# Kernel tuning notes

Measured on AMD Instinct MI355X. Metric: run time of the kernel, lower is better.

The kernel has to match this reference:

```python
import jax, jax.numpy as jnp
import numpy as np

IN_SHAPE = 640
LEVELS = [3, 4, 5]          # pyramid_levels [3,5] expanded
REG_LEN = 64
NUM_CLASSES = 80
MAX_OUT = 100
SCORE_TH = 0.3
IOU_TH = 0.5
NEG_INF = -1e30


def _make_anchors():
    """Anchor-free anchors: one box per grid cell, grid_zero_start=True,
    anchor_scale=1, aspect_ratio=1 -> half-size = stride/2. Normalized by input size."""
    all_a = []
    for lvl in LEVELS:
        stride = 2 ** lvl
        fs = IN_SHAPE // stride
        hh = np.arange(fs, dtype='float32') * stride
        ww = np.arange(fs, dtype='float32') * stride
        wg, hg = np.meshgrid(ww, hh)
        centers = np.stack([hg, wg], -1).reshape(-1, 2)  # [fs*fs, 2] (h, w)
        half = stride * 0.5
        all_a.append(np.concatenate([centers - half, centers + half], -1))
    return np.concatenate(all_a, 0) / IN_SHAPE  # [8400, 4]


def setup_inputs() -> dict:
    key = jax.random.key(0)
    preds = jax.random.normal(key, (64, 8400, REG_LEN + NUM_CLASSES), dtype=jnp.float32)
    anchors = jnp.asarray(_make_anchors(), dtype=jnp.float32)
    return {"preds": preds, "anchors": anchors}


def _decode_yolov8(preds, anchors):
    bbox_logits, cls_logits = preds[..., :REG_LEN], preds[..., REG_LEN:]
    B, N = bbox_logits.shape[:2]
    bins = REG_LEN // 4  # 16
    d = bbox_logits.reshape(B, N, 4, bins)
    # softmax-weighted DFL expectation over bins
    d = jnp.sum(jax.nn.softmax(d, axis=-1) * jnp.arange(bins, dtype=d.dtype), axis=-1)  # [B,N,4]
    tl, br = d[..., :2], d[..., 2:]
    anchors_hw = anchors[:, 2:] - anchors[:, :2]          # [N,2]
    anchors_ctr = (anchors[:, :2] + anchors[:, 2:]) * 0.5  # [N,2]
    bc = (br - tl) * 0.5 * anchors_hw + anchors_ctr        # center
    bhw = (br + tl) * anchors_hw                           # height/width
    boxes = jnp.concatenate([bc - bhw * 0.5, bc + bhw * 0.5], -1)  # [B,N,4] corners
    return boxes, cls_logits


def _iou_one_vs_all(box, boxes):
    tl = jnp.maximum(box[:2], boxes[:, :2])
    br = jnp.minimum(box[2:], boxes[:, 2:])
    inter = jnp.prod(jnp.clip(br - tl, 0.0, None), -1)
    a1 = jnp.prod(box[2:] - box[:2])
    a2 = jnp.prod(boxes[:, 2:] - boxes[:, :2], -1)
    return inter / (a1 + a2 - inter + 1e-9)


def _nms_single(boxes, scores):
    """Greedy hard NMS for one image. boxes [N,4], scores [N] -> idxs [MAX_OUT] (-1 = invalid)."""
    n = scores.shape[0]
    sc0 = jnp.where(scores > SCORE_TH, scores, NEG_INF)

    def step(sc, _):
        j = jnp.argmax(sc)
        valid = sc[j] > NEG_INF * 0.5
        idx = jnp.where(valid, j, -1).astype(jnp.int32)
        iou = _iou_one_vs_all(boxes[j], boxes)
        sc = jnp.where((iou > IOU_TH) | (jnp.arange(n) == j), NEG_INF, sc)
        return sc, idx

    _, idxs = jax.lax.scan(step, sc0, None, length=MAX_OUT)
    return idxs


def reference(preds, anchors):
    boxes, cls = _decode_yolov8(preds, anchors)       # [B,N,4], [B,N,C]
    scores = jnp.max(cls, -1)                          # [B,N]
    labels = jnp.argmax(cls, -1).astype(jnp.int32)     # [B,N]
    idxs = jax.vmap(_nms_single)(boxes, scores)        # [B,MAX_OUT]
    valid = idxs >= 0
    safe = jnp.maximum(idxs, 0)
    out_boxes = jnp.take_along_axis(boxes, safe[:, :, None], axis=1) * valid[..., None]
    out_scores = jnp.take_along_axis(scores, safe, axis=1) * valid
    out_labels = jnp.where(valid, jnp.take_along_axis(labels, safe, axis=1), -1)
    return out_boxes, out_labels, out_scores
```

## Files before the change

kernel.cpp:

```cpp
#include <hip/hip_runtime.h>

namespace {
constexpr int kB = 64;
constexpr int kN = 8400;
constexpr int kMain = 8192;
constexpr int kTail = kN - kMain;
constexpr int kReg = 64;
constexpr int kCls = 80;
constexpr int kStride = kReg + kCls;
constexpr int kMaxOut = 100;
constexpr float kScoreTh = 0.3f;
constexpr float kIouTh = 0.5f;
}

__global__ __launch_bounds__(256) void decode2_k(
    const float* __restrict__ preds,
    const float* __restrict__ anchors,
    float4* __restrict__ boxes,
    float* __restrict__ scores,
    int* __restrict__ labels,
    unsigned long long* __restrict__ keys)
{
    __shared__ float lds[64 * 148];
    const int tid = threadIdx.x;
    const size_t gbase = (size_t)blockIdx.x * 64;

    const float4* src = (const float4*)(preds + gbase * kStride);
    float4* l4 = (float4*)lds;
#pragma unroll
    for (int k = 0; k < 9; ++k) {
        int i = tid + k * 256;
        int row = i / 36, col = i - row * 36;
        l4[row * 37 + col] = src[i];
    }
    __syncthreads();

    const int a = tid >> 2, s = tid & 3;
    const float* rowp = lds + a * 148;

    float x[16];
    const float4* q = (const float4*)(rowp + s * 16);
#pragma unroll
    for (int j = 0; j < 4; ++j) ((float4*)x)[j] = q[j];
    float m = x[0];
#pragma unroll
    for (int j = 1; j < 16; ++j) m = fmaxf(m, x[j]);
    float se = 0.f, we = 0.f;
#pragma unroll
    for (int j = 0; j < 16; ++j) {
        float t = expf(x[j] - m);
        se += t;
        we += t * (float)j;
    }
    float d = we / se;

    const float4* cl = (const float4*)(rowp + kReg + s * 20);
    float bv = -3e38f; int bi = 0;
#pragma unroll
    for (int c = 0; c < 5; ++c) {
        float4 v = cl[c];
        int cb = s * 20 + 4 * c;
        if (v.x > bv) { bv = v.x; bi = cb; }
        if (v.y > bv) { bv = v.y; bi = cb + 1; }
        if (v.z > bv) { bv = v.z; bi = cb + 2; }
        if (v.w > bv) { bv = v.w; bi = cb + 3; }
    }

    const int lane = tid & 63;
    const int base = lane & ~3;
    float d0 = __shfl(d, base + 0, 64);
    float d1 = __shfl(d, base + 1, 64);
    float d2 = __shfl(d, base + 2, 64);
    float d3 = __shfl(d, base + 3, 64);
    float v1 = __shfl(bv, base + 1, 64); int i1 = __shfl(bi, base + 1, 64);
    float v2 = __shfl(bv, base + 2, 64); int i2 = __shfl(bi, base + 2, 64);
    float v3 = __shfl(bv, base + 3, 64); int i3 = __shfl(bi, base + 3, 64);

    if (s == 0) {
        float best = bv; int bl = bi;
        if (v1 > best) { best = v1; bl = i1; }
        if (v2 > best) { best = v2; bl = i2; }
        if (v3 > best) { best = v3; bl = i3; }

        size_t gi = gbase + a;
        int bimg = (int)(gi / kN);
        int n = (int)(gi - (size_t)bimg * kN);
        float4 av = ((const float4*)anchors)[n];
        float ah0 = av.z - av.x, ah1 = av.w - av.y;
        float c0 = (av.x + av.z) * 0.5f, c1 = (av.y + av.w) * 0.5f;
        float bc0 = (d2 - d0) * 0.5f * ah0 + c0;
        float bc1 = (d3 - d1) * 0.5f * ah1 + c1;
        float bh0 = (d2 + d0) * ah0;
        float bh1 = (d3 + d1) * ah1;
        boxes[gi] = make_float4(bc0 - bh0 * 0.5f, bc1 - bh1 * 0.5f,
                                bc0 + bh0 * 0.5f, bc1 + bh1 * 0.5f);
        scores[gi] = best;
        labels[gi] = bl;

        unsigned long long kkey = ~0ULL;
        if (best > kScoreTh) {
            unsigned u = __float_as_uint(best);
            unsigned o = u ^ ((u & 0x80000000u) ? 0xFFFFFFFFu : 0x80000000u);
            kkey = ((unsigned long long)(~o) << 32) | (unsigned)n;
        }
        keys[((size_t)bimg << 14) + n] = kkey;
    }
}

__global__ __launch_bounds__(512) void sortL_k(unsigned long long* __restrict__ keys)
{
    __shared__ unsigned long long lk[2048];
    const int img = blockIdx.x >> 2, seg = blockIdx.x & 3;
    const int gofs = seg << 11;
    unsigned long long* base = keys + ((size_t)img << 14) + gofs;

    for (int t = threadIdx.x; t < 2048; t += 512) lk[t] = base[t];
    __syncthreads();
    for (int size = 2; size <= 2048; size <<= 1) {
        for (int stride = size >> 1; stride > 0; stride >>= 1) {
#pragma unroll
            for (int p = 0; p < 2; ++p) {
                int n = threadIdx.x + (p << 9);
                int i = ((n & ~(stride - 1)) << 1) | (n & (stride - 1));
                int j = i + stride;
                bool desc = ((gofs + i) & size) != 0;
                unsigned long long a = lk[i], c = lk[j];
                bool sw = desc ? (c > a) : (a > c);
                if (sw) { lk[i] = c; lk[j] = a; }
            }
            __syncthreads();
        }
    }
    for (int t = threadIdx.x; t < 2048; t += 512) base[t] = lk[t];
}

__global__ __launch_bounds__(256) void gce_k(unsigned long long* __restrict__ keys)
{
    int tg = blockIdx.x * 256 + threadIdx.x;
    int img = tg >> 12;
    int n = tg & 4095;
    unsigned long long* base = keys + ((size_t)img << 14);
    unsigned long long a = base[n], c = base[n + 4096];
    if (a > c) { base[n] = c; base[n + 4096] = a; }
}

template <int SIZE>
__global__ __launch_bounds__(512) void lm2_k(unsigned long long* __restrict__ keys)
{
    __shared__ unsigned long long lk[4096];
    const int img = blockIdx.x >> 1, half = blockIdx.x & 1;
    const int gofs = half << 12;
    unsigned long long* base = keys + ((size_t)img << 14) + gofs;

    for (int t = threadIdx.x; t < 4096; t += 512) lk[t] = base[t];
    __syncthreads();
    const bool desc = (gofs & SIZE) != 0;
    for (int stride = 2048; stride > 0; stride >>= 1) {
#pragma unroll
        for (int p = 0; p < 4; ++p) {
            int n = threadIdx.x + (p << 9);
            int i = ((n & ~(stride - 1)) << 1) | (n & (stride - 1));
            int j = i + stride;
            unsigned long long a = lk[i], c = lk[j];
            bool sw = desc ? (c > a) : (a > c);
            if (sw) { lk[i] = c; lk[j] = a; }
        }
        __syncthreads();
    }
    for (int t = threadIdx.x; t < 4096; t += 512) base[t] = lk[t];
}

__device__ __forceinline__ unsigned long long getB_(
    const unsigned long long* tailL, int p1, int x)
{
    int t = p1 + x;
    return (t < 256) ? tailL[t] : ~0ULL;
}

__global__ __launch_bounds__(256) void nms_k(
    const float4* __restrict__ boxes,
    const float* __restrict__ scores,
    const int* __restrict__ labels,
    const unsigned long long* __restrict__ keys,
    float* __restrict__ out)
{
    __shared__ unsigned long long tailL[256];
    __shared__ unsigned long long aw[512];
    __shared__ float4 sbox[256];
    __shared__ float  sar[256];
    __shared__ int    sidx[256];
    __shared__ float4 kboxL[kMaxOut];
    __shared__ float  kareaL[kMaxOut];
    __shared__ int    kidxL[kMaxOut];
    __shared__ unsigned long long ballS[4];
    __shared__ int p0S, p1S, kcS, doneS, stopS;

    const int b = blockIdx.x, tid = threadIdx.x;
    const unsigned long long* mainA = keys + ((size_t)b << 14);
    const float4* bx = boxes + (size_t)b * kN;

    if (tid == 0) { p0S = 0; p1S = 0; kcS = 0; doneS = 0; }

    tailL[tid] = (tid < kTail) ? mainA[kMain + tid] : ~0ULL;
    __syncthreads();
    for (int size = 2; size <= 256; size <<= 1) {
        for (int stride = size >> 1; stride > 0; stride >>= 1) {
            if (tid < 128) {
                int i = ((tid & ~(stride - 1)) << 1) | (tid & (stride - 1));
                int j = i + stride;
                bool desc = (i & size) != 0;
                unsigned long long a = tailL[i], c = tailL[j];
                bool sw = desc ? (c > a) : (a > c);
                if (sw) { tailL[i] = c; tailL[j] = a; }
            }
            __syncthreads();
        }
    }

    int kc = 0;
    for (int c = 0; c < 33; ++c) {
        int p0 = p0S, p1 = p1S;
        aw[tid]       = (p0 + tid       < kMain) ? mainA[p0 + tid]       : ~0ULL;
        aw[tid + 256] = (p0 + tid + 256 < kMain) ? mainA[p0 + tid + 256] : ~0ULL;
        __syncthreads();

        int d = tid;
        int lo = 0, hi = d;
        while (lo < hi) {
            int mid = (lo + hi) >> 1;
            bool c2 = getB_(tailL, p1, d - mid - 1) < aw[mid];
            if (c2) hi = mid; else lo = mid + 1;
        }
        unsigned long long av = aw[lo];
        unsigned long long bv = getB_(tailL, p1, d - lo);
        unsigned long long key = (av <= bv) ? av : bv;

        bool alive = (key != ~0ULL);
        int idx = alive ? (int)(key & 0xFFFFFFFFULL) : 0;
        float4 cb = bx[idx];
        float ac = (cb.z - cb.x) * (cb.w - cb.y);

        if (alive) {
            for (int k = 0; k < kc; ++k) {
                float4 kb = kboxL[k];
                float t0 = fmaxf(kb.x, cb.x), t1 = fmaxf(kb.y, cb.y);
                float b0 = fminf(kb.z, cb.z), b1 = fminf(kb.w, cb.w);
                float inter = fmaxf(b0 - t0, 0.f) * fmaxf(b1 - t1, 0.f);
                float iou = inter / (kareaL[k] + ac - inter + 1e-9f);
                if (iou > kIouTh) { alive = false; break; }
            }
        }
        sbox[tid] = cb; sar[tid] = ac; sidx[tid] = idx;
        unsigned long long mm = __ballot((int)alive);
        if ((tid & 63) == 0) ballS[tid >> 6] = mm;
        if (tid == 0) {
            stopS = (key == ~0ULL);
            int lo2 = 0, hi2 = 256;
            while (lo2 < hi2) {
                int mid = (lo2 + hi2) >> 1;
                bool c2 = getB_(tailL, p1, 255 - mid) < aw[mid];
                if (c2) hi2 = mid; else lo2 = mid + 1;
            }
            p0S = p0 + lo2; p1S = p1 + (256 - lo2);
        }
        __syncthreads();
        if (stopS) break;

        if (tid < 64) {
            const int lane = tid;
            unsigned a4 = 0;
#pragma unroll
            for (int j = 0; j < 4; ++j)
                a4 |= (unsigned)((ballS[j] >> lane) & 1ULL) << j;
            int kcl = kc;
            while (true) {
                int jF = -1, lF = 0;
#pragma unroll
                for (int j = 0; j < 4; ++j) {
                    if (jF < 0) {
                        unsigned long long m2 = __ballot((int)((a4 >> j) & 1u));
                        if (m2) { jF = j; lF = __ffsll((unsigned long long)m2) - 1; }
                    }
                }
                if (jF < 0) break;
                int cs = (jF << 6) + lF;
                float4 kb = sbox[cs];
                float kar = sar[cs];
                if (lane == 0) {
                    kboxL[kcl] = kb; kareaL[kcl] = kar; kidxL[kcl] = sidx[cs];
                }
                if (lane == lF) a4 &= ~(1u << jF);
                ++kcl;
                if (kcl == kMaxOut) break;
#pragma unroll
                for (int j = 0; j < 4; ++j) {
                    if ((a4 >> j) & 1u) {
                        float4 cb2 = sbox[lane + (j << 6)];
                        float ac2 = sar[lane + (j << 6)];
                        float t0 = fmaxf(kb.x, cb2.x), t1 = fmaxf(kb.y, cb2.y);
                        float b0 = fminf(kb.z, cb2.z), b1 = fminf(kb.w, cb2.w);
                        float inter = fmaxf(b0 - t0, 0.f) * fmaxf(b1 - t1, 0.f);
                        float iou = inter / (kar + ac2 - inter + 1e-9f);
                        if (iou > kIouTh) a4 &= ~(1u << j);
                    }
                }
            }
            if (lane == 0) { kcS = kcl; if (kcl == kMaxOut) doneS = 1; }
        }
        __syncthreads();
        kc = kcS;
        if (doneS) break;
    }

    int kcf = kcS;
    if (tid < kMaxOut) {
        if (tid < kcf) {
            int idx = kidxL[tid];
            ((float4*)out)[b * kMaxOut + tid] = kboxL[tid];
            out[kB * kMaxOut * 4 + b * kMaxOut + tid] =
                (float)labels[(size_t)b * kN + idx];
            out[kB * kMaxOut * 5 + b * kMaxOut + tid] =
                scores[(size_t)b * kN + idx];
        } else {
            ((float4*)out)[b * kMaxOut + tid] = make_float4(0.f, 0.f, 0.f, 0.f);
            out[kB * kMaxOut * 4 + b * kMaxOut + tid] = -1.0f;
            out[kB * kMaxOut * 5 + b * kMaxOut + tid] = 0.0f;
        }
    }
}

extern "C" void kernel_launch(void* const* d_in, const int* in_sizes, int n_in,
                              void* d_out, int out_size, void* d_ws, size_t ws_size,
                              hipStream_t stream)
{
    const float* preds = (const float*)d_in[0];
    const float* anchors = (const float*)d_in[1];
    float* out = (float*)d_out;

    char* ws = (char*)d_ws;
    float4* boxes = (float4*)ws;
    float* scores = (float*)(ws + (size_t)kB * kN * 16);
    int* labels = (int*)(ws + (size_t)kB * kN * 20);
    unsigned long long* keys =
        (unsigned long long*)(ws + (size_t)kB * kN * 24);

    decode2_k<<<(kB * kN) / 64, 256, 0, stream>>>(preds, anchors, boxes, scores, labels, keys);
    sortL_k<<<kB * 4, 512, 0, stream>>>(keys);
    lm2_k<4096><<<kB * 2, 512, 0, stream>>>(keys);
    gce_k<<<(kB * 4096) / 256, 256, 0, stream>>>(keys);
    lm2_k<8192><<<kB * 2, 512, 0, stream>>>(keys);
    nms_k<<<kB, 256, 0, stream>>>(boxes, scores, labels, keys, out);
}
```

Measured before the change: 512.8 us.

## Precompute merged sorted keys and widen NMS to 512-candidate chunks

The final global compare-exchange step is folded into the last bitonic merge kernel, so one launch is removed. The tail merge with the 208 leftover keys moves out of the NMS loop into a separate merge-path kernel that writes a fully sorted key array. NMS then reads 512 candidates per chunk with 512 threads and no per-chunk binary search. The wave-level suppression uses an 8-bit mask per lane with padded shared-memory layout and a shuffle to find the next keeper. This costs an extra workspace buffer and an extra global pass over the keys.

```diff
diff --git a/kernel.cpp b/kernel.cpp
--- a/kernel.cpp
+++ b/kernel.cpp
@@ -9,6 +9,7 @@
 constexpr int kCls = 80;
 constexpr int kStride = kReg + kCls;
 constexpr int kMaxOut = 100;
+constexpr int kM2 = 8704;
 constexpr float kScoreTh = 0.3f;
 constexpr float kIouTh = 0.5f;
 }
@@ -134,18 +135,7 @@
     for (int t = threadIdx.x; t < 2048; t += 512) base[t] = lk[t];
 }
 
-__global__ __launch_bounds__(256) void gce_k(unsigned long long* __restrict__ keys)
-{
-    int tg = blockIdx.x * 256 + threadIdx.x;
-    int img = tg >> 12;
-    int n = tg & 4095;
-    unsigned long long* base = keys + ((size_t)img << 14);
-    unsigned long long a = base[n], c = base[n + 4096];
-    if (a > c) { base[n] = c; base[n + 4096] = a; }
-}
-
-template <int SIZE>
-__global__ __launch_bounds__(512) void lm2_k(unsigned long long* __restrict__ keys)
+__global__ __launch_bounds__(512) void lm4_k(unsigned long long* __restrict__ keys)
 {
     __shared__ unsigned long long lk[4096];
     const int img = blockIdx.x >> 1, half = blockIdx.x & 1;
@@ -154,7 +144,7 @@
 
     for (int t = threadIdx.x; t < 4096; t += 512) lk[t] = base[t];
     __syncthreads();
-    const bool desc = (gofs & SIZE) != 0;
+    const bool desc = (gofs & 4096) != 0;
     for (int stride = 2048; stride > 0; stride >>= 1) {
 #pragma unroll
         for (int p = 0; p < 4; ++p) {
@@ -170,38 +160,46 @@
     for (int t = threadIdx.x; t < 4096; t += 512) base[t] = lk[t];
 }
 
-__device__ __forceinline__ unsigned long long getB_(
-    const unsigned long long* tailL, int p1, int x)
-{
-    int t = p1 + x;
-    return (t < 256) ? tailL[t] : ~0ULL;
-}
-
-__global__ __launch_bounds__(256) void nms_k(
-    const float4* __restrict__ boxes,
-    const float* __restrict__ scores,
-    const int* __restrict__ labels,
+__global__ __launch_bounds__(512) void lm8f_k(
     const unsigned long long* __restrict__ keys,
-    float* __restrict__ out)
+    unsigned long long* __restrict__ keysM)
+{
+    __shared__ unsigned long long lk[4096];
+    const int img = blockIdx.x >> 1, half = blockIdx.x & 1;
+    const unsigned long long* base = keys + ((size_t)img << 14);
+
+    for (int t = threadIdx.x; t < 4096; t += 512) {
+        unsigned long long a = base[t], c = base[t + 4096];
+        lk[t] = half ? (a > c ? a : c) : (a > c ? c : a);
+    }
+    __syncthreads();
+    for (int stride = 2048; stride > 0; stride >>= 1) {
+#pragma unroll
+        for (int p = 0; p < 4; ++p) {
+            int n = threadIdx.x + (p << 9);
+            int i = ((n & ~(stride - 1)) << 1) | (n & (stride - 1));
+            int j = i + stride;
+            unsigned long long a = lk[i], c = lk[j];
+            if (a > c) { lk[i] = c; lk[j] = a; }
+        }
+        __syncthreads();
+    }
+    unsigned long long* dst = keysM + ((size_t)img << 13) + ((size_t)half << 12);
+    for (int t = threadIdx.x; t < 4096; t += 512) dst[t] = lk[t];
+}
+
+__global__ __launch_bounds__(512) void mergeT_k(
+    const unsigned long long* __restrict__ keysM,
+    const unsigned long long* __restrict__ keys,
+    unsigned long long* __restrict__ keys2)
 {
     __shared__ unsigned long long tailL[256];
-    __shared__ unsigned long long aw[512];
-    __shared__ float4 sbox[256];
-    __shared__ float  sar[256];
-    __shared__ int    sidx[256];
-    __shared__ float4 kboxL[kMaxOut];
-    __shared__ float  kareaL[kMaxOut];
-    __shared__ int    kidxL[kMaxOut];
-    __shared__ unsigned long long ballS[4];
-    __shared__ int p0S, p1S, kcS, doneS, stopS;
-
     const int b = blockIdx.x, tid = threadIdx.x;
-    const unsigned long long* mainA = keys + ((size_t)b << 14);
-    const float4* bx = boxes + (size_t)b * kN;
-
-    if (tid == 0) { p0S = 0; p1S = 0; kcS = 0; doneS = 0; }
-
-    tailL[tid] = (tid < kTail) ? mainA[kMain + tid] : ~0ULL;
+    const unsigned long long* A = keysM + ((size_t)b << 13);
+    unsigned long long* dst = keys2 + (size_t)b * kM2;
+
+    if (tid < 256)
+        tailL[tid] = (tid < kTail) ? keys[((size_t)b << 14) + kMain + tid] : ~0ULL;
     __syncthreads();
     for (int size = 2; size <= 256; size <<= 1) {
         for (int stride = size >> 1; stride > 0; stride >>= 1) {
@@ -217,24 +215,49 @@
         }
     }
 
+    const int d0 = tid * 17;
+    int lo = d0 - 256; lo = lo < 0 ? 0 : (lo > kMain ? kMain : lo);
+    int hi = d0 > kMain ? kMain : d0;
+    while (lo < hi) {
+        int mid = (lo + hi) >> 1;
+        if (tailL[d0 - mid - 1] < A[mid]) hi = mid; else lo = mid + 1;
+    }
+    int ai = lo, bi = d0 - lo;
+#pragma unroll
+    for (int k = 0; k < 17; ++k) {
+        unsigned long long av = (ai < kMain) ? A[ai] : ~0ULL;
+        unsigned long long bv = (bi < 256) ? tailL[bi] : ~0ULL;
+        unsigned long long v;
+        if (av <= bv) { v = av; ++ai; } else { v = bv; ++bi; }
+        dst[d0 + k] = v;
+    }
+}
+
+__global__ __launch_bounds__(512) void nms_k(
+    const float4* __restrict__ boxes,
+    const float* __restrict__ scores,
+    const int* __restrict__ labels,
+    const unsigned long long* __restrict__ keys2,
+    float* __restrict__ out)
+{
+    __shared__ float4 sboxT[576];
+    __shared__ float  sarT[576];
+    __shared__ int    sidxT[576];
+    __shared__ float4 kboxL[kMaxOut];
+    __shared__ float  kareaL[kMaxOut];
+    __shared__ int    kidxL[kMaxOut];
+    __shared__ unsigned long long ballS[8];
+    __shared__ int kcS, doneS, stopS;
+
+    const int b = blockIdx.x, tid = threadIdx.x;
+    const unsigned long long* src = keys2 + (size_t)b * kM2;
+    const float4* bx = boxes + (size_t)b * kN;
+
+    if (tid == 0) { kcS = 0; doneS = 0; }
+
     int kc = 0;
-    for (int c = 0; c < 33; ++c) {
-        int p0 = p0S, p1 = p1S;
-        aw[tid]       = (p0 + tid       < kMain) ? mainA[p0 + tid]       : ~0ULL;
-        aw[tid + 256] = (p0 + tid + 256 < kMain) ? mainA[p0 + tid + 256] : ~0ULL;
-        __syncthreads();
-
-        int d = tid;
-        int lo = 0, hi = d;
-        while (lo < hi) {
-            int mid = (lo + hi) >> 1;
-            bool c2 = getB_(tailL, p1, d - mid - 1) < aw[mid];
-            if (c2) hi = mid; else lo = mid + 1;
-        }
-        unsigned long long av = aw[lo];
-        unsigned long long bv = getB_(tailL, p1, d - lo);
-        unsigned long long key = (av <= bv) ? av : bv;
-
+    for (int c = 0; c < 17; ++c) {
+        unsigned long long key = src[(c << 9) + tid];
         bool alive = (key != ~0ULL);
         int idx = alive ? (int)(key & 0xFFFFFFFFULL) : 0;
         float4 cb = bx[idx];
@@ -250,62 +273,46 @@
                 if (iou > kIouTh) { alive = false; break; }
             }
         }
-        sbox[tid] = cb; sar[tid] = ac; sidx[tid] = idx;
+        const int sl = ((tid >> 3) * 9) + (tid & 7);
+        sboxT[sl] = cb; sarT[sl] = ac; sidxT[sl] = idx;
         unsigned long long mm = __ballot((int)alive);
         if ((tid & 63) == 0) ballS[tid >> 6] = mm;
-        if (tid == 0) {
-            stopS = (key == ~0ULL);
-            int lo2 = 0, hi2 = 256;
-            while (lo2 < hi2) {
-                int mid = (lo2 + hi2) >> 1;
-                bool c2 = getB_(tailL, p1, 255 - mid) < aw[mid];
-                if (c2) hi2 = mid; else lo2 = mid + 1;
-            }
-            p0S = p0 + lo2; p1S = p1 + (256 - lo2);
-        }
+        if (tid == 0) stopS = (key == ~0ULL);
         __syncthreads();
         if (stopS) break;
 
         if (tid < 64) {
-            const int lane = tid;
-            unsigned a4 = 0;
-#pragma unroll
-            for (int j = 0; j < 4; ++j)
-                a4 |= (unsigned)((ballS[j] >> lane) & 1ULL) << j;
+            const int l = tid;
+            unsigned a8 = (unsigned)((ballS[l >> 3] >> ((l & 7) << 3)) & 0xFFULL);
             int kcl = kc;
             while (true) {
-                int jF = -1, lF = 0;
-#pragma unroll
-                for (int j = 0; j < 4; ++j) {
-                    if (jF < 0) {
-                        unsigned long long m2 = __ballot((int)((a4 >> j) & 1u));
-                        if (m2) { jF = j; lF = __ffsll((unsigned long long)m2) - 1; }
-                    }
-                }
-                if (jF < 0) break;
-                int cs = (jF << 6) + lF;
-                float4 kb = sbox[cs];
-                float kar = sar[cs];
-                if (lane == 0) {
-                    kboxL[kcl] = kb; kareaL[kcl] = kar; kidxL[kcl] = sidx[cs];
-                }
-                if (lane == lF) a4 &= ~(1u << jF);
+                unsigned long long m = __ballot(a8 != 0);
+                if (!m) break;
+                int lf = __ffsll(m) - 1;
+                unsigned af = (unsigned)__shfl((int)a8, lf, 64);
+                int jf = __ffs((int)af) - 1;
+                int ks = lf * 9 + jf;
+                float4 kb = sboxT[ks];
+                float kar = sarT[ks];
+                if (l == 0) { kboxL[kcl] = kb; kareaL[kcl] = kar; kidxL[kcl] = sidxT[ks]; }
+                if (l == lf) a8 &= ~(1u << jf);
                 ++kcl;
                 if (kcl == kMaxOut) break;
 #pragma unroll
-                for (int j = 0; j < 4; ++j) {
-                    if ((a4 >> j) & 1u) {
-                        float4 cb2 = sbox[lane + (j << 6)];
-                        float ac2 = sar[lane + (j << 6)];
+                for (int j = 0; j < 8; ++j) {
+                    if ((a8 >> j) & 1u) {
+                        int sj = l * 9 + j;
+                        float4 cb2 = sboxT[sj];
+                        float ac2 = sarT[sj];
                         float t0 = fmaxf(kb.x, cb2.x), t1 = fmaxf(kb.y, cb2.y);
                         float b0 = fminf(kb.z, cb2.z), b1 = fminf(kb.w, cb2.w);
                         float inter = fmaxf(b0 - t0, 0.f) * fmaxf(b1 - t1, 0.f);
                         float iou = inter / (kar + ac2 - inter + 1e-9f);
-                        if (iou > kIouTh) a4 &= ~(1u << j);
+                        if (iou > kIouTh) a8 &= ~(1u << j);
                     }
                 }
             }
-            if (lane == 0) { kcS = kcl; if (kcl == kMaxOut) doneS = 1; }
+            if (l == 0) { kcS = kcl; if (kcl == kMaxOut) doneS = 1; }
         }
         __syncthreads();
         kc = kcS;
@@ -343,11 +350,14 @@
     int* labels = (int*)(ws + (size_t)kB * kN * 20);
     unsigned long long* keys =
         (unsigned long long*)(ws + (size_t)kB * kN * 24);
+    unsigned long long* keysM =
+        (unsigned long long*)(ws + (size_t)kB * kN * 24 + (size_t)kB * 16384 * 8);
+    unsigned long long* keys2 = keysM + (size_t)kB * kMain;
 
     decode2_k<<<(kB * kN) / 64, 256, 0, stream>>>(preds, anchors, boxes, scores, labels, keys);
     sortL_k<<<kB * 4, 512, 0, stream>>>(keys);
-    lm2_k<4096><<<kB * 2, 512, 0, stream>>>(keys);
-    gce_k<<<(kB * 4096) / 256, 256, 0, stream>>>(keys);
-    lm2_k<8192><<<kB * 2, 512, 0, stream>>>(keys);
-    nms_k<<<kB, 256, 0, stream>>>(boxes, scores, labels, keys, out);
-}
+    lm4_k<<<kB * 2, 512, 0, stream>>>(keys);
+    lm8f_k<<<kB * 2, 512, 0, stream>>>(keys, keysM);
+    mergeT_k<<<kB, 512, 0, stream>>>(keysM, keys, keys2);
+    nms_k<<<kB, 512, 0, stream>>>(boxes, scores, labels, keys2, out);
+}
```

Measured after the change: 565.1 us. +10.2%, slower.

## Keep bitonic sort keys in registers with wave shuffles and LDS exchange

Applied to the files above, without the earlier changes.

The bitonic sort and merge kernels now keep 4 or 8 keys per thread in registers. Strides within a thread are handled in registers, strides within a wavefront use __shfl_xor, and only large strides exchange through LDS, each with a pair of barriers. This removes most LDS traffic and the barrier after every stride. The cost is higher register pressure and more complex index logic that has to match the original sort direction exactly.

```diff
diff --git a/kernel.cpp b/kernel.cpp
--- a/kernel.cpp
+++ b/kernel.cpp
@@ -110,28 +110,71 @@
 __global__ __launch_bounds__(512) void sortL_k(unsigned long long* __restrict__ keys)
 {
     __shared__ unsigned long long lk[2048];
+    const int tid = threadIdx.x;
     const int img = blockIdx.x >> 2, seg = blockIdx.x & 3;
     const int gofs = seg << 11;
     unsigned long long* base = keys + ((size_t)img << 14) + gofs;
 
-    for (int t = threadIdx.x; t < 2048; t += 512) lk[t] = base[t];
-    __syncthreads();
-    for (int size = 2; size <= 2048; size <<= 1) {
-        for (int stride = size >> 1; stride > 0; stride >>= 1) {
-#pragma unroll
-            for (int p = 0; p < 2; ++p) {
-                int n = threadIdx.x + (p << 9);
-                int i = ((n & ~(stride - 1)) << 1) | (n & (stride - 1));
-                int j = i + stride;
-                bool desc = ((gofs + i) & size) != 0;
-                unsigned long long a = lk[i], c = lk[j];
-                bool sw = desc ? (c > a) : (a > c);
-                if (sw) { lk[i] = c; lk[j] = a; }
+    unsigned long long r[4];
+    const int e0 = tid << 2;
+#pragma unroll
+    for (int k = 0; k < 4; ++k) r[k] = base[e0 + k];
+
+    auto ce2 = [&](int size) {
+#pragma unroll
+        for (int k = 0; k < 2; ++k) {
+            bool desc = (((gofs + e0 + k) & size) != 0);
+            unsigned long long a = r[k], c = r[k + 2];
+            bool sw = desc ? (c > a) : (a > c);
+            if (sw) { r[k] = c; r[k + 2] = a; }
+        }
+    };
+    auto ce1 = [&](int size) {
+#pragma unroll
+        for (int k = 0; k < 4; k += 2) {
+            bool desc = (((gofs + e0 + k) & size) != 0);
+            unsigned long long a = r[k], c = r[k + 1];
+            bool sw = desc ? (c > a) : (a > c);
+            if (sw) { r[k] = c; r[k + 1] = a; }
+        }
+    };
+
+    ce1(2);
+    for (int size = 4; size <= 2048; size <<= 1) {
+        for (int stride = size >> 1; stride >= 4; stride >>= 1) {
+            if (stride >= 256) {
+                __syncthreads();
+#pragma unroll
+                for (int k = 0; k < 4; ++k) lk[k * 512 + tid] = r[k];
+                __syncthreads();
+                const int pt = tid ^ (stride >> 2);
+#pragma unroll
+                for (int k = 0; k < 4; ++k) {
+                    unsigned long long o = lk[k * 512 + pt];
+                    int e = e0 + k;
+                    bool keep_min = (((e & stride) == 0) !=
+                                     (((gofs + e) & size) != 0));
+                    r[k] = keep_min ? (r[k] < o ? r[k] : o)
+                                    : (r[k] > o ? r[k] : o);
+                }
+            } else {
+                const int d = stride >> 2;
+#pragma unroll
+                for (int k = 0; k < 4; ++k) {
+                    unsigned long long o = __shfl_xor(r[k], d, 64);
+                    int e = e0 + k;
+                    bool keep_min = (((e & stride) == 0) !=
+                                     (((gofs + e) & size) != 0));
+                    r[k] = keep_min ? (r[k] < o ? r[k] : o)
+                                    : (r[k] > o ? r[k] : o);
+                }
             }
-            __syncthreads();
-        }
-    }
-    for (int t = threadIdx.x; t < 2048; t += 512) base[t] = lk[t];
+        }
+        ce2(size);
+        ce1(size);
+    }
+#pragma unroll
+    for (int k = 0; k < 4; ++k) base[e0 + k] = r[k];
 }
 
 __global__ __launch_bounds__(256) void gce_k(unsigned long long* __restrict__ keys)
@@ -148,26 +191,49 @@
 __global__ __launch_bounds__(512) void lm2_k(unsigned long long* __restrict__ keys)
 {
     __shared__ unsigned long long lk[4096];
+    const int tid = threadIdx.x;
     const int img = blockIdx.x >> 1, half = blockIdx.x & 1;
     const int gofs = half << 12;
     unsigned long long* base = keys + ((size_t)img << 14) + gofs;
-
-    for (int t = threadIdx.x; t < 4096; t += 512) lk[t] = base[t];
-    __syncthreads();
     const bool desc = (gofs & SIZE) != 0;
-    for (int stride = 2048; stride > 0; stride >>= 1) {
-#pragma unroll
-        for (int p = 0; p < 4; ++p) {
-            int n = threadIdx.x + (p << 9);
-            int i = ((n & ~(stride - 1)) << 1) | (n & (stride - 1));
-            int j = i + stride;
-            unsigned long long a = lk[i], c = lk[j];
-            bool sw = desc ? (c > a) : (a > c);
-            if (sw) { lk[i] = c; lk[j] = a; }
-        }
+
+    unsigned long long r[8];
+    const int e0 = tid << 3;
+#pragma unroll
+    for (int k = 0; k < 8; ++k) r[k] = base[e0 + k];
+
+    for (int stride = 2048; stride >= 512; stride >>= 1) {
         __syncthreads();
-    }
-    for (int t = threadIdx.x; t < 4096; t += 512) base[t] = lk[t];
+#pragma unroll
+        for (int k = 0; k < 8; ++k) lk[k * 512 + tid] = r[k];
+        __syncthreads();
+        const int pt = tid ^ (stride >> 3);
+#pragma unroll
+        for (int k = 0; k < 8; ++k) {
+            unsigned long long o = lk[k * 512 + pt];
+            bool keep_min = ((((e0 + k) & stride) == 0) != desc);
+            r[k] = keep_min ? (r[k] < o ? r[k] : o) : (r[k] > o ? r[k] : o);
+        }
+    }
+    for (int stride = 256; stride >= 8; stride >>= 1) {
+        const int d = stride >> 3;
+#pragma unroll
+        for (int k = 0; k < 8; ++k) {
+            unsigned long long o = __shfl_xor(r[k], d, 64);
+            bool keep_min = ((((e0 + k) & stride) == 0) != desc);
+            r[k] = keep_min ? (r[k] < o ? r[k] : o) : (r[k] > o ? r[k] : o);
+        }
+    }
+    auto ce = [&](int i, int j) {
+        unsigned long long a = r[i], c = r[j];
+        bool sw = desc ? (c > a) : (a > c);
+        if (sw) { r[i] = c; r[j] = a; }
+    };
+    ce(0, 4); ce(1, 5); ce(2, 6); ce(3, 7);
+    ce(0, 2); ce(1, 3); ce(4, 6); ce(5, 7);
+    ce(0, 1); ce(2, 3); ce(4, 5); ce(6, 7);
+#pragma unroll
+    for (int k = 0; k < 8; ++k) base[e0 + k] = r[k];
 }
 
 __device__ __forceinline__ unsigned long long getB_(
```

Measured after the change: 509.3 us. Within noise of the previous version (-0.7%).
